# Kernel tuning notes

Hardware: AMD Instinct MI355X
Metric: run time of the kernel (lower is better)

Reference implementation:

```python
import jax, jax.numpy as jnp
import numpy as np

NUM_QUERIES = 300


def setup_inputs() -> dict:
    key = jax.random.key(0)
    ks = jax.random.split(key, 16)
    B, C, NC = 16, 256, 80
    s = 0.02
    return {
        "s3": jax.random.normal(ks[0], (B, C, 128, 128), jnp.float32),
        "s4": jax.random.normal(ks[1], (B, C, 64, 64), jnp.float32),
        "s5": jax.random.normal(ks[2], (B, C, 32, 32), jnp.float32),
        "w_score": jax.random.normal(ks[3], (C, NC), jnp.float32) * s,
        "b_score": jnp.zeros((NC,), jnp.float32),
        "w1": jax.random.normal(ks[4], (C, C), jnp.float32) * s,
        "b1": jnp.zeros((C,), jnp.float32),
        "w2": jax.random.normal(ks[5], (C, C), jnp.float32) * s,
        "b2": jnp.zeros((C,), jnp.float32),
        "w3": jax.random.normal(ks[6], (C, 4), jnp.float32) * s,
        "b3": jnp.zeros((4,), jnp.float32),
        "w_proj": jax.random.normal(ks[7], (C, C), jnp.float32) * s,
        "b_proj": jnp.zeros((C,), jnp.float32),
    }


def _flatten(feats):
    # each feat [B,C,H,W] -> [B,H*W,C]; concat over levels
    mems = [f.reshape(f.shape[0], f.shape[1], -1).transpose(0, 2, 1) for f in feats]
    return jnp.concatenate(mems, axis=1)


def reference(s3, s4, s5, w_score, b_score, w1, b1, w2, b2, w3, b3, w_proj, b_proj):
    memory = _flatten([s3, s4, s5])  # [B, N, C]

    # encoder heads
    enc_logits = memory @ w_score + b_score                      # [B, N, num_classes]
    h = jax.nn.relu(memory @ w1 + b1)
    h = jax.nn.relu(h @ w2 + b2)
    enc_boxes = h @ w3 + b3                                      # [B, N, 4]

    # top-k query selection: sigmoid -> per-token max class score -> topk -> gather
    scores = jax.nn.sigmoid(enc_logits).max(axis=-1)             # [B, N]
    topk_scores, topk_idx = jax.lax.top_k(scores, NUM_QUERIES)   # [B, K]
    topk_mem = jnp.take_along_axis(memory, topk_idx[:, :, None], axis=1)    # [B, K, C]
    topk_boxes = jnp.take_along_axis(enc_boxes, topk_idx[:, :, None], axis=1)  # [B, K, 4]

    tgt = topk_mem @ w_proj + b_proj                             # [B, K, C]
    ref_points = jax.nn.sigmoid(topk_boxes)                      # [B, K, 4]

    return (tgt, ref_points, enc_logits, jax.nn.sigmoid(enc_boxes), topk_idx, topk_scores)
```

## Files before the change

### kernel.cpp

```cpp
#include <hip/hip_runtime.h>
#include <math.h>

#define BATCH 16
#define CDIM 256
#define NCLS 80
#define N3 16384
#define N4 4096
#define N5 1024
#define NTOK 21504
#define KQ 300
#define KSEL 512
#define CANDMAX 1024

typedef __attribute__((ext_vector_type(8))) short short8;
typedef __attribute__((ext_vector_type(4))) float floatx4;
typedef unsigned short ushort_t;

__device__ __forceinline__ float sigmoidf_(float x) {
    return 1.0f / (1.0f + __expf(-x));
}

__device__ __forceinline__ ushort_t f2bf(float f) {
    unsigned int x = __float_as_uint(f);
    unsigned int r = (x + 0x7FFFu + ((x >> 16) & 1u)) >> 16;
    return (ushort_t)r;
}

__device__ __forceinline__ void locate_level(
    int n, int bb,
    const float* __restrict__ s3, const float* __restrict__ s4, const float* __restrict__ s5,
    const float*& src, int& nloc, int& lsz)
{
    if (n < N3)           { src = s3 + (size_t)bb * CDIM * N3; nloc = n;           lsz = N3; }
    else if (n < N3 + N4) { src = s4 + (size_t)bb * CDIM * N4; nloc = n - N3;      lsz = N4; }
    else                  { src = s5 + (size_t)bb * CDIM * N5; nloc = n - N3 - N4; lsz = N5; }
}

__global__ __launch_bounds__(256) void prep_weights(
    const float* __restrict__ w1, const float* __restrict__ w2,
    const float* __restrict__ w_score,
    ushort_t* __restrict__ w1T, ushort_t* __restrict__ w2T, ushort_t* __restrict__ wsT)
{
    const int k = threadIdx.x;
    const int c = blockIdx.x;
    if (c < 256) {
        w1T[c * 256 + k] = f2bf(w1[k * 256 + c]);
    } else if (c < 512) {
        const int c2 = c - 256;
        w2T[c2 * 256 + k] = f2bf(w2[k * 256 + c2]);
    } else {
        const int c2 = c - 512;
        wsT[c2 * 256 + k] = (c2 < NCLS) ? f2bf(w_score[k * NCLS + c2]) : (ushort_t)0;
    }
}

__global__ __launch_bounds__(256, 3) void enc_mfma_kernel(
    const float* __restrict__ s3, const float* __restrict__ s4, const float* __restrict__ s5,
    const ushort_t* __restrict__ w1T, const ushort_t* __restrict__ w2T,
    const ushort_t* __restrict__ wsT,
    const float* __restrict__ b_score, const float* __restrict__ b1,
    const float* __restrict__ b2,
    const float* __restrict__ w3, const float* __restrict__ b3,
    float* __restrict__ out_logits, float* __restrict__ out_sboxes,
    float* __restrict__ ws_scores)
{
    __shared__ __align__(16) ushort_t ldsA[256 * 68];
    __shared__ __align__(16) ushort_t wbuf[32][264];

    const int t = threadIdx.x;
    const int lane = t & 63;
    const int w = t >> 6;
    const int ml = lane & 15;
    const int quad = lane >> 4;
    const int kq = quad * 8;

    const int bb = blockIdx.x / 336;
    const int tile = blockIdx.x % 336;
    const int T0 = tile * 64;

    const float* src; int nloc, lsz;
    locate_level(T0, bb, s3, s4, s5, src, nloc, lsz);

    {
        const int tokq = t & 15;
        const int kr = t >> 4;
        #pragma unroll
        for (int p = 0; p < 16; ++p) {
            const int k = p * 16 + kr;
            const float4 v = *(const float4*)(src + (size_t)k * lsz + nloc + 4 * tokq);
            const unsigned int lo = (unsigned int)f2bf(v.x) | ((unsigned int)f2bf(v.y) << 16);
            const unsigned int hi = (unsigned int)f2bf(v.z) | ((unsigned int)f2bf(v.w) << 16);
            *(uint2*)&ldsA[k * 68 + 4 * tokq] = make_uint2(lo, hi);
        }
    }
    __syncthreads();

    short8 af[8];
    #pragma unroll
    for (int f = 0; f < 8; ++f) {
        short8 a;
        #pragma unroll
        for (int j = 0; j < 8; ++j)
            a[j] = (short)ldsA[(32 * f + kq + j) * 68 + 16 * w + ml];
        af[f] = a;
    }

    auto stage_w = [&](const ushort_t* wg) {
        #pragma unroll
        for (int s2 = 0; s2 < 4; ++s2) {
            const int idx = s2 * 256 + t;
            const int col = idx >> 5, ks = idx & 31;
            const short8 v = *(const short8*)(wg + (size_t)col * 256 + ks * 8);
            *(short8*)&wbuf[col][ks * 8] = v;
        }
    };

    const int tokg0 = bb * NTOK + T0 + 16 * w + quad * 4;
    const int tokl0 = 16 * w + quad * 4;

    float smax[4] = {-1e30f, -1e30f, -1e30f, -1e30f};
    for (int cc = 0; cc < 3; ++cc) {
        __syncthreads();
        stage_w(wsT + (size_t)cc * 32 * 256);
        __syncthreads();
        #pragma unroll
        for (int tt = 0; tt < 2; ++tt) {
            const int gt = cc * 2 + tt;
            if (gt >= 5) continue;
            floatx4 acc = {0.f, 0.f, 0.f, 0.f};
            #pragma unroll
            for (int f = 0; f < 8; ++f) {
                const short8 bf = *(const short8*)&wbuf[16 * tt + ml][32 * f + kq];
                acc = __builtin_amdgcn_mfma_f32_16x16x32_bf16(af[f], bf, acc, 0, 0, 0);
            }
            const int col = 16 * gt + ml;
            const float bias = b_score[col];
            #pragma unroll
            for (int r = 0; r < 4; ++r) {
                const float v = acc[r] + bias;
                out_logits[(size_t)(tokg0 + r) * NCLS + col] = v;
                smax[r] = fmaxf(smax[r], v);
            }
        }
    }
    #pragma unroll
    for (int r = 0; r < 4; ++r) {
        float m = smax[r];
        m = fmaxf(m, __shfl_xor(m, 1));
        m = fmaxf(m, __shfl_xor(m, 2));
        m = fmaxf(m, __shfl_xor(m, 4));
        m = fmaxf(m, __shfl_xor(m, 8));
        smax[r] = m;
    }
    if (ml == 0) {
        #pragma unroll
        for (int r = 0; r < 4; ++r)
            ws_scores[bb * NTOK + T0 + 16 * w + quad * 4 + r] = sigmoidf_(smax[r]);
    }

    for (int cc = 0; cc < 8; ++cc) {
        __syncthreads();
        stage_w(w1T + (size_t)cc * 32 * 256);
        __syncthreads();
        #pragma unroll
        for (int tt = 0; tt < 2; ++tt) {
            floatx4 acc = {0.f, 0.f, 0.f, 0.f};
            #pragma unroll
            for (int f = 0; f < 8; ++f) {
                const short8 bf = *(const short8*)&wbuf[16 * tt + ml][32 * f + kq];
                acc = __builtin_amdgcn_mfma_f32_16x16x32_bf16(af[f], bf, acc, 0, 0, 0);
            }
            const int col = 32 * cc + 16 * tt + ml;
            const float bias = b1[col];
            #pragma unroll
            for (int r = 0; r < 4; ++r) {
                const float v = fmaxf(acc[r] + bias, 0.f);
                ldsA[(tokl0 + r) * 264 + col] = f2bf(v);
            }
        }
    }
    __syncthreads();

    #pragma unroll
    for (int f = 0; f < 8; ++f)
        af[f] = *(const short8*)&ldsA[(16 * w + ml) * 264 + 32 * f + kq];

    float psum[4][4];
    #pragma unroll
    for (int r = 0; r < 4; ++r)
        #pragma unroll
        for (int c = 0; c < 4; ++c) psum[r][c] = 0.f;

    for (int cc = 0; cc < 8; ++cc) {
        __syncthreads();
        stage_w(w2T + (size_t)cc * 32 * 256);
        __syncthreads();
        #pragma unroll
        for (int tt = 0; tt < 2; ++tt) {
            floatx4 acc = {0.f, 0.f, 0.f, 0.f};
            #pragma unroll
            for (int f = 0; f < 8; ++f) {
                const short8 bf = *(const short8*)&wbuf[16 * tt + ml][32 * f + kq];
                acc = __builtin_amdgcn_mfma_f32_16x16x32_bf16(af[f], bf, acc, 0, 0, 0);
            }
            const int col = 32 * cc + 16 * tt + ml;
            const float bias = b2[col];
            const float4 w3v = *(const float4*)(w3 + col * 4);
            #pragma unroll
            for (int r = 0; r < 4; ++r) {
                const float v = fmaxf(acc[r] + bias, 0.f);
                psum[r][0] = fmaf(v, w3v.x, psum[r][0]);
                psum[r][1] = fmaf(v, w3v.y, psum[r][1]);
                psum[r][2] = fmaf(v, w3v.z, psum[r][2]);
                psum[r][3] = fmaf(v, w3v.w, psum[r][3]);
            }
        }
    }
    #pragma unroll
    for (int r = 0; r < 4; ++r)
        #pragma unroll
        for (int c = 0; c < 4; ++c) {
            float v = psum[r][c];
            v += __shfl_xor(v, 1);
            v += __shfl_xor(v, 2);
            v += __shfl_xor(v, 4);
            v += __shfl_xor(v, 8);
            psum[r][c] = v;
        }
    if (ml == 0) {
        #pragma unroll
        for (int r = 0; r < 4; ++r) {
            float4 o;
            o.x = sigmoidf_(psum[r][0] + b3[0]);
            o.y = sigmoidf_(psum[r][1] + b3[1]);
            o.z = sigmoidf_(psum[r][2] + b3[2]);
            o.w = sigmoidf_(psum[r][3] + b3[3]);
            *(float4*)&out_sboxes[(size_t)(bb * NTOK + T0 + 16 * w + quad * 4 + r) * 4] = o;
        }
    }
}

__global__ __launch_bounds__(256) void select_kernel(
    const float* __restrict__ scores,
    int* __restrict__ cand_idx, unsigned int* __restrict__ cand_cnt)
{
    const int bb = blockIdx.x;
    const int t = threadIdx.x;
    const float* s = scores + bb * NTOK;

    __shared__ unsigned int hist[256];
    __shared__ unsigned int prefix_s, cnt_s;

    unsigned int prefix = 0, mask = 0;
    int remaining = KSEL;
    for (int pass = 0; pass < 4; pass++) {
        const int shift = 24 - 8 * pass;
        hist[t] = 0;
        __syncthreads();
        for (int n = t; n < NTOK; n += 256) {
            unsigned int key = __float_as_uint(s[n]);
            if ((key & mask) == prefix) atomicAdd(&hist[(key >> shift) & 255u], 1u);
        }
        __syncthreads();
        if (t == 0) {
            int rem = remaining; unsigned int bsel = 0;
            for (int bin = 255; bin >= 0; bin--) {
                int c = (int)hist[bin];
                if (c >= rem) { bsel = (unsigned int)bin; break; }
                rem -= c;
            }
            prefix_s = prefix | (bsel << shift);
            hist[255] = (unsigned int)rem;
        }
        __syncthreads();
        prefix = prefix_s; remaining = (int)hist[255];
        mask |= 0xFFu << shift;
        __syncthreads();
    }
    const unsigned int Tkey = prefix;

    if (t == 0) cnt_s = 0;
    __syncthreads();
    for (int n = t; n < NTOK; n += 256) {
        unsigned int key = __float_as_uint(s[n]);
        if (key >= Tkey) {
            unsigned int pos = atomicAdd(&cnt_s, 1u);
            if (pos < CANDMAX) cand_idx[bb * CANDMAX + pos] = n;
        }
    }
    __syncthreads();
    if (t == 0) {
        unsigned int c = cnt_s; if (c > CANDMAX) c = CANDMAX;
        cand_cnt[bb] = c;
    }
}

__global__ __launch_bounds__(256) void rescore_kernel(
    const float* __restrict__ s3, const float* __restrict__ s4, const float* __restrict__ s5,
    const float* __restrict__ w_score, const float* __restrict__ b_score,
    const int* __restrict__ cand_idx, const unsigned int* __restrict__ cand_cnt,
    double* __restrict__ cand_score)
{
    __shared__ float mrow[4][CDIM];
    const int t = threadIdx.x;
    const int w = t >> 6;
    const int lane = t & 63;
    const int bb = blockIdx.x / (CANDMAX / 4);
    const int c  = (blockIdx.x % (CANDMAX / 4)) * 4 + w;
    const unsigned int cnt = cand_cnt[bb];
    const bool active = (unsigned int)c < cnt;

    int n = 0;
    if (active) n = cand_idx[bb * CANDMAX + c];
    if (active) {
        const float* src; int nloc, lsz;
        locate_level(n, bb, s3, s4, s5, src, nloc, lsz);
        #pragma unroll
        for (int j = 0; j < 4; j++)
            mrow[w][4 * lane + j] = src[(size_t)(4 * lane + j) * lsz + nloc];
    }
    __syncthreads();

    if (active) {
        double acc0 = (double)b_score[lane];
        double acc1 = (lane < 16) ? (double)b_score[64 + lane] : -1.0e300;
        for (int k = 0; k < CDIM; k++) {
            const double m = (double)mrow[w][k];
            acc0 += m * (double)w_score[k * NCLS + lane];
            if (lane < 16) acc1 += m * (double)w_score[k * NCLS + 64 + lane];
        }
        double mx = fmax(acc0, acc1);
        mx = fmax(mx, __shfl_xor(mx, 1));
        mx = fmax(mx, __shfl_xor(mx, 2));
        mx = fmax(mx, __shfl_xor(mx, 4));
        mx = fmax(mx, __shfl_xor(mx, 8));
        mx = fmax(mx, __shfl_xor(mx, 16));
        mx = fmax(mx, __shfl_xor(mx, 32));
        if (lane == 0) cand_score[bb * CANDMAX + c] = mx;
    }
}

__global__ __launch_bounds__(256) void fsort_kernel(
    const double* __restrict__ cand_score, const int* __restrict__ cand_idx,
    const unsigned int* __restrict__ cand_cnt,
    float* __restrict__ out_idx_f, float* __restrict__ out_scores,
    int* __restrict__ ws_idx)
{
    __shared__ double ss[CANDMAX];
    __shared__ int    ii[CANDMAX];
    const int bb = blockIdx.x;
    const int t = threadIdx.x;
    const unsigned int cnt = cand_cnt[bb];

    for (int i = t; i < CANDMAX; i += 256) {
        if ((unsigned int)i < cnt) {
            ss[i] = cand_score[bb * CANDMAX + i];
            ii[i] = cand_idx[bb * CANDMAX + i];
        } else {
            ss[i] = -1.0e300;
            ii[i] = 0x7FFFFFFF;
        }
    }
    __syncthreads();

    for (int ksz = 2; ksz <= CANDMAX; ksz <<= 1) {
        for (int j = ksz >> 1; j > 0; j >>= 1) {
            #pragma unroll
            for (int p = 0; p < CANDMAX / 256; p++) {
                const int i = p * 256 + t;
                const int ixj = i ^ j;
                if (ixj > i) {
                    double sa = ss[i], sb = ss[ixj];
                    int ia = ii[i], ib = ii[ixj];
                    const bool up = ((i & ksz) != 0);
                    const bool agtb = (sa > sb) || (sa == sb && ia < ib);
                    if (agtb == up) { ss[i] = sb; ss[ixj] = sa; ii[i] = ib; ii[ixj] = ia; }
                }
            }
            __syncthreads();
        }
    }

    for (int q = t; q < KQ; q += 256) {
        const double x = ss[q];
        const int idx = ii[q];
        out_scores[bb * KQ + q] = (float)(1.0 / (1.0 + exp(-x)));
        out_idx_f[bb * KQ + q] = (float)idx;
        ws_idx[bb * KQ + q] = idx;
    }
}

__global__ __launch_bounds__(256) void gather_proj_kernel(
    const float* __restrict__ s3, const float* __restrict__ s4, const float* __restrict__ s5,
    const float* __restrict__ w_proj, const float* __restrict__ b_proj,
    const int* __restrict__ ws_idx, const float* __restrict__ out_sboxes,
    float* __restrict__ out_tgt, float* __restrict__ out_ref)
{
    __shared__ float memQ[20][CDIM];
    __shared__ int qidx[20];
    const int t = threadIdx.x;
    const int bb = blockIdx.x / 15;
    const int tile = blockIdx.x % 15;
    const int q0 = tile * 20;

    if (t < 20) qidx[t] = ws_idx[bb * KQ + q0 + t];
    __syncthreads();

    #pragma unroll 4
    for (int q = 0; q < 20; q++) {
        const int n = qidx[q];
        const float* src; int nloc, lsz;
        locate_level(n, bb, s3, s4, s5, src, nloc, lsz);
        memQ[q][t] = src[(size_t)t * lsz + nloc];
    }
    __syncthreads();

    const int j = t;
    float acc[20];
    #pragma unroll
    for (int q = 0; q < 20; q++) acc[q] = b_proj[j];
    for (int k = 0; k < CDIM; k++) {
        const float w = w_proj[(size_t)k * CDIM + j];
        #pragma unroll
        for (int q = 0; q < 20; q++) acc[q] = fmaf(memQ[q][k], w, acc[q]);
    }
    #pragma unroll
    for (int q = 0; q < 20; q++)
        out_tgt[(size_t)(bb * KQ + q0 + q) * CDIM + j] = acc[q];

    if (t < 80) {
        const int q = t >> 2, c = t & 3;
        const int n = qidx[q];
        out_ref[(size_t)(bb * KQ + q0 + q) * 4 + c] =
            out_sboxes[(size_t)(bb * NTOK + n) * 4 + c];
    }
}

extern "C" void kernel_launch(void* const* d_in, const int* in_sizes, int n_in,
                              void* d_out, int out_size, void* d_ws, size_t ws_size,
                              hipStream_t stream) {
    const float* s3      = (const float*)d_in[0];
    const float* s4      = (const float*)d_in[1];
    const float* s5      = (const float*)d_in[2];
    const float* w_score = (const float*)d_in[3];
    const float* b_score = (const float*)d_in[4];
    const float* w1      = (const float*)d_in[5];
    const float* b1      = (const float*)d_in[6];
    const float* w2      = (const float*)d_in[7];
    const float* b2      = (const float*)d_in[8];
    const float* w3      = (const float*)d_in[9];
    const float* b3      = (const float*)d_in[10];
    const float* w_proj  = (const float*)d_in[11];
    const float* b_proj  = (const float*)d_in[12];

    float* out = (float*)d_out;
    float* out_tgt    = out;
    float* out_ref    = out + 1228800;
    float* out_logits = out + 1248000;
    float* out_sboxes = out + 28773120;
    float* out_idx    = out + 30149376;
    float* out_scores = out + 30154176;

    char* ws = (char*)d_ws;
    float*        ws_scores  = (float*)(ws + 0);
    double*       cand_score = (double*)(ws + 1376256);
    int*          cand_idx   = (int*)(ws + 1507328);
    unsigned int* cand_cnt   = (unsigned int*)(ws + 1572864);
    int*          ws_idx     = (int*)(ws + 1573120);
    ushort_t*     w1T        = (ushort_t*)(ws + 1592576);
    ushort_t*     w2T        = (ushort_t*)(ws + 1723648);
    ushort_t*     wsT        = (ushort_t*)(ws + 1854720);

    prep_weights<<<608, 256, 0, stream>>>(w1, w2, w_score, w1T, w2T, wsT);

    enc_mfma_kernel<<<BATCH * 336, 256, 0, stream>>>(
        s3, s4, s5, w1T, w2T, wsT, b_score, b1, b2, w3, b3,
        out_logits, out_sboxes, ws_scores);

    select_kernel<<<BATCH, 256, 0, stream>>>(ws_scores, cand_idx, cand_cnt);

    rescore_kernel<<<BATCH * (CANDMAX / 4), 256, 0, stream>>>(
        s3, s4, s5, w_score, b_score, cand_idx, cand_cnt, cand_score);

    fsort_kernel<<<BATCH, 256, 0, stream>>>(
        cand_score, cand_idx, cand_cnt, out_idx, out_scores, ws_idx);

    gather_proj_kernel<<<BATCH * 15, 256, 0, stream>>>(
        s3, s4, s5, w_proj, b_proj, ws_idx, out_sboxes, out_tgt, out_ref);
}
```

Before: 952.0 us.

## Double-buffer weight staging with async global-to-LDS loads and speed up selection

The encoder kernel now merges its three weight loops into one 19-step pipeline. It stages the next 32-column weight chunk into a second LDS buffer with global_load_lds while the current chunk feeds the MFMAs, and pre-swizzles the transposed weights to avoid LDS bank conflicts. Biases and w3 are cached in LDS, and the launch-bounds occupancy hint drops from 3 to 2 because LDS use grows. Separately, select_kernel moves to 1024 threads and uses wave-aggregated ballot atomics for the histogram and compaction. The candidate compaction order may now differ from before.

```diff
diff --git a/kernel.cpp b/kernel.cpp
--- a/kernel.cpp
+++ b/kernel.cpp
@@ -26,6 +26,13 @@
     return (ushort_t)r;
 }
 
+__device__ __forceinline__ void gload16(const void* g, void* l) {
+    __builtin_amdgcn_global_load_lds(
+        (const __attribute__((address_space(1))) unsigned int*)g,
+        (__attribute__((address_space(3))) unsigned int*)l,
+        16, 0, 0);
+}
+
 __device__ __forceinline__ void locate_level(
     int n, int bb,
     const float* __restrict__ s3, const float* __restrict__ s4, const float* __restrict__ s5,
@@ -43,18 +50,22 @@
 {
     const int k = threadIdx.x;
     const int c = blockIdx.x;
+    const int klo = k & 7;
     if (c < 256) {
-        w1T[c * 256 + k] = f2bf(w1[k * 256 + c]);
+        const size_t d = (size_t)c * 256 + ((((k >> 3) ^ (c & 7)) << 3) | klo);
+        w1T[d] = f2bf(w1[k * 256 + c]);
     } else if (c < 512) {
         const int c2 = c - 256;
-        w2T[c2 * 256 + k] = f2bf(w2[k * 256 + c2]);
+        const size_t d = (size_t)c2 * 256 + ((((k >> 3) ^ (c2 & 7)) << 3) | klo);
+        w2T[d] = f2bf(w2[k * 256 + c2]);
     } else {
         const int c2 = c - 512;
-        wsT[c2 * 256 + k] = (c2 < NCLS) ? f2bf(w_score[k * NCLS + c2]) : (ushort_t)0;
-    }
-}
-
-__global__ __launch_bounds__(256, 3) void enc_mfma_kernel(
+        const size_t d = (size_t)c2 * 256 + ((((k >> 3) ^ (c2 & 7)) << 3) | klo);
+        wsT[d] = (c2 < NCLS) ? f2bf(w_score[k * NCLS + c2]) : (ushort_t)0;
+    }
+}
+
+__global__ __launch_bounds__(256, 2) void enc_mfma_kernel(
     const float* __restrict__ s3, const float* __restrict__ s4, const float* __restrict__ s5,
     const ushort_t* __restrict__ w1T, const ushort_t* __restrict__ w2T,
     const ushort_t* __restrict__ wsT,
@@ -65,7 +76,11 @@
     float* __restrict__ ws_scores)
 {
     __shared__ __align__(16) ushort_t ldsA[256 * 68];
-    __shared__ __align__(16) ushort_t wbuf[32][264];
+    __shared__ __align__(16) ushort_t wbufL[2][32 * 256];
+    __shared__ float bsc_s[96];
+    __shared__ float b1_s[256];
+    __shared__ float b2_s[256];
+    __shared__ __align__(16) float w3_s[256 * 4];
 
     const int t = threadIdx.x;
     const int lane = t & 63;
@@ -73,10 +88,26 @@
     const int ml = lane & 15;
     const int quad = lane >> 4;
     const int kq = quad * 8;
+    const int m8 = ml & 7;
 
     const int bb = blockIdx.x / 336;
     const int tile = blockIdx.x % 336;
     const int T0 = tile * 64;
+
+    auto stage_async = [&](const ushort_t* wg, int dbuf) {
+        const char* g = (const char*)wg + w * 1024 + (lane << 4);
+        char* l = (char*)&wbufL[dbuf][0] + w * 1024;
+        #pragma unroll
+        for (int i = 0; i < 4; ++i)
+            gload16(g + i * 4096, l + i * 4096);
+    };
+
+    stage_async(wsT, 0);
+
+    if (t < 96) bsc_s[t] = b_score[t];
+    b1_s[t] = b1[t];
+    b2_s[t] = b2[t];
+    *(float4*)&w3_s[t * 4] = *(const float4*)(w3 + t * 4);
 
     const float* src; int nloc, lsz;
     locate_level(T0, bb, s3, s4, s5, src, nloc, lsz);
@@ -105,117 +136,96 @@
         af[f] = a;
     }
 
-    auto stage_w = [&](const ushort_t* wg) {
-        #pragma unroll
-        for (int s2 = 0; s2 < 4; ++s2) {
-            const int idx = s2 * 256 + t;
-            const int col = idx >> 5, ks = idx & 31;
-            const short8 v = *(const short8*)(wg + (size_t)col * 256 + ks * 8);
-            *(short8*)&wbuf[col][ks * 8] = v;
-        }
-    };
-
-    const int tokg0 = bb * NTOK + T0 + 16 * w + quad * 4;
     const int tokl0 = 16 * w + quad * 4;
+    const int tokg0 = bb * NTOK + T0 + tokl0;
 
     float smax[4] = {-1e30f, -1e30f, -1e30f, -1e30f};
-    for (int cc = 0; cc < 3; ++cc) {
-        __syncthreads();
-        stage_w(wsT + (size_t)cc * 32 * 256);
-        __syncthreads();
+    float psum[4][4];
+    #pragma unroll
+    for (int r = 0; r < 4; ++r)
+        #pragma unroll
+        for (int c = 0; c < 4; ++c) psum[r][c] = 0.f;
+
+    int cur = 0;
+    for (int i = 0; i < 19; ++i) {
+        if (i + 1 < 19) {
+            const int j = i + 1;
+            const ushort_t* nxt = (j < 3)  ? (wsT + (size_t)j * 8192)
+                                : (j < 11) ? (w1T + (size_t)(j - 3) * 8192)
+                                           : (w2T + (size_t)(j - 11) * 8192);
+            stage_async(nxt, cur ^ 1);
+        }
+
+        if (i == 11) {
+            #pragma unroll
+            for (int f = 0; f < 8; ++f)
+                af[f] = *(const short8*)&ldsA[(16 * w + ml) * 264 + 32 * f + kq];
+        }
+
+        const ushort_t* wb = &wbufL[cur][0];
         #pragma unroll
         for (int tt = 0; tt < 2; ++tt) {
-            const int gt = cc * 2 + tt;
-            if (gt >= 5) continue;
+            if (i < 3 && (2 * i + tt) >= 5) continue;
+            const int row = 16 * tt + ml;
             floatx4 acc = {0.f, 0.f, 0.f, 0.f};
             #pragma unroll
             for (int f = 0; f < 8; ++f) {
-                const short8 bf = *(const short8*)&wbuf[16 * tt + ml][32 * f + kq];
+                const short8 bf = *(const short8*)&wb[row * 256 + (((4 * f + quad) ^ m8) << 3)];
                 acc = __builtin_amdgcn_mfma_f32_16x16x32_bf16(af[f], bf, acc, 0, 0, 0);
             }
-            const int col = 16 * gt + ml;
-            const float bias = b_score[col];
+            if (i < 3) {
+                const int col = 16 * (2 * i + tt) + ml;
+                const float bias = bsc_s[col];
+                #pragma unroll
+                for (int r = 0; r < 4; ++r) {
+                    const float v = acc[r] + bias;
+                    out_logits[(size_t)(tokg0 + r) * NCLS + col] = v;
+                    smax[r] = fmaxf(smax[r], v);
+                }
+            } else if (i < 11) {
+                const int col = 32 * (i - 3) + 16 * tt + ml;
+                const float bias = b1_s[col];
+                #pragma unroll
+                for (int r = 0; r < 4; ++r) {
+                    const float v = fmaxf(acc[r] + bias, 0.f);
+                    ldsA[(tokl0 + r) * 264 + col] = f2bf(v);
+                }
+            } else {
+                const int col = 32 * (i - 11) + 16 * tt + ml;
+                const float bias = b2_s[col];
+                const float4 w3v = *(const float4*)&w3_s[col * 4];
+                #pragma unroll
+                for (int r = 0; r < 4; ++r) {
+                    const float v = fmaxf(acc[r] + bias, 0.f);
+                    psum[r][0] = fmaf(v, w3v.x, psum[r][0]);
+                    psum[r][1] = fmaf(v, w3v.y, psum[r][1]);
+                    psum[r][2] = fmaf(v, w3v.z, psum[r][2]);
+                    psum[r][3] = fmaf(v, w3v.w, psum[r][3]);
+                }
+            }
+        }
+
+        if (i == 2) {
             #pragma unroll
             for (int r = 0; r < 4; ++r) {
-                const float v = acc[r] + bias;
-                out_logits[(size_t)(tokg0 + r) * NCLS + col] = v;
-                smax[r] = fmaxf(smax[r], v);
-            }
-        }
-    }
-    #pragma unroll
-    for (int r = 0; r < 4; ++r) {
-        float m = smax[r];
-        m = fmaxf(m, __shfl_xor(m, 1));
-        m = fmaxf(m, __shfl_xor(m, 2));
-        m = fmaxf(m, __shfl_xor(m, 4));
-        m = fmaxf(m, __shfl_xor(m, 8));
-        smax[r] = m;
-    }
-    if (ml == 0) {
-        #pragma unroll
-        for (int r = 0; r < 4; ++r)
-            ws_scores[bb * NTOK + T0 + 16 * w + quad * 4 + r] = sigmoidf_(smax[r]);
-    }
-
-    for (int cc = 0; cc < 8; ++cc) {
+                float m = smax[r];
+                m = fmaxf(m, __shfl_xor(m, 1));
+                m = fmaxf(m, __shfl_xor(m, 2));
+                m = fmaxf(m, __shfl_xor(m, 4));
+                m = fmaxf(m, __shfl_xor(m, 8));
+                smax[r] = m;
+            }
+            if (ml == 0) {
+                #pragma unroll
+                for (int r = 0; r < 4; ++r)
+                    ws_scores[bb * NTOK + T0 + 16 * w + quad * 4 + r] = sigmoidf_(smax[r]);
+            }
+        }
+
         __syncthreads();
-        stage_w(w1T + (size_t)cc * 32 * 256);
-        __syncthreads();
-        #pragma unroll
-        for (int tt = 0; tt < 2; ++tt) {
-            floatx4 acc = {0.f, 0.f, 0.f, 0.f};
-            #pragma unroll
-            for (int f = 0; f < 8; ++f) {
-                const short8 bf = *(const short8*)&wbuf[16 * tt + ml][32 * f + kq];
-                acc = __builtin_amdgcn_mfma_f32_16x16x32_bf16(af[f], bf, acc, 0, 0, 0);
-            }
-            const int col = 32 * cc + 16 * tt + ml;
-            const float bias = b1[col];
-            #pragma unroll
-            for (int r = 0; r < 4; ++r) {
-                const float v = fmaxf(acc[r] + bias, 0.f);
-                ldsA[(tokl0 + r) * 264 + col] = f2bf(v);
-            }
-        }
-    }
-    __syncthreads();
-
-    #pragma unroll
-    for (int f = 0; f < 8; ++f)
-        af[f] = *(const short8*)&ldsA[(16 * w + ml) * 264 + 32 * f + kq];
-
-    float psum[4][4];
-    #pragma unroll
-    for (int r = 0; r < 4; ++r)
-        #pragma unroll
-        for (int c = 0; c < 4; ++c) psum[r][c] = 0.f;
-
-    for (int cc = 0; cc < 8; ++cc) {
-        __syncthreads();
-        stage_w(w2T + (size_t)cc * 32 * 256);
-        __syncthreads();
-        #pragma unroll
-        for (int tt = 0; tt < 2; ++tt) {
-            floatx4 acc = {0.f, 0.f, 0.f, 0.f};
-            #pragma unroll
-            for (int f = 0; f < 8; ++f) {
-                const short8 bf = *(const short8*)&wbuf[16 * tt + ml][32 * f + kq];
-                acc = __builtin_amdgcn_mfma_f32_16x16x32_bf16(af[f], bf, acc, 0, 0, 0);
-            }
-            const int col = 32 * cc + 16 * tt + ml;
-            const float bias = b2[col];
-            const float4 w3v = *(const float4*)(w3 + col * 4);
-            #pragma unroll
-            for (int r = 0; r < 4; ++r) {
-                const float v = fmaxf(acc[r] + bias, 0.f);
-                psum[r][0] = fmaf(v, w3v.x, psum[r][0]);
-                psum[r][1] = fmaf(v, w3v.y, psum[r][1]);
-                psum[r][2] = fmaf(v, w3v.z, psum[r][2]);
-                psum[r][3] = fmaf(v, w3v.w, psum[r][3]);
-            }
-        }
-    }
+        cur ^= 1;
+    }
+
     #pragma unroll
     for (int r = 0; r < 4; ++r)
         #pragma unroll
@@ -240,26 +250,37 @@
     }
 }
 
-__global__ __launch_bounds__(256) void select_kernel(
+__global__ __launch_bounds__(1024) void select_kernel(
     const float* __restrict__ scores,
     int* __restrict__ cand_idx, unsigned int* __restrict__ cand_cnt)
 {
     const int bb = blockIdx.x;
     const int t = threadIdx.x;
+    const int lane = t & 63;
     const float* s = scores + bb * NTOK;
 
     __shared__ unsigned int hist[256];
-    __shared__ unsigned int prefix_s, cnt_s;
+    __shared__ unsigned int prefix_s, rem_s, cnt_s;
 
     unsigned int prefix = 0, mask = 0;
     int remaining = KSEL;
     for (int pass = 0; pass < 4; pass++) {
         const int shift = 24 - 8 * pass;
-        hist[t] = 0;
+        if (t < 256) hist[t] = 0;
         __syncthreads();
-        for (int n = t; n < NTOK; n += 256) {
-            unsigned int key = __float_as_uint(s[n]);
-            if ((key & mask) == prefix) atomicAdd(&hist[(key >> shift) & 255u], 1u);
+        for (int n = t; n < NTOK; n += 1024) {
+            const unsigned int key = __float_as_uint(s[n]);
+            const bool pred = ((key & mask) == prefix);
+            const unsigned int bin = (key >> shift) & 255u;
+            unsigned long long alive = __ballot(pred);
+            while (alive) {
+                const int leader = __builtin_ctzll(alive);
+                const unsigned int lbin = (unsigned int)__shfl((int)bin, leader);
+                const unsigned long long match = alive & __ballot(bin == lbin);
+                if (lane == leader)
+                    atomicAdd(&hist[lbin], (unsigned int)__popcll(match));
+                alive &= ~match;
+            }
         }
         __syncthreads();
         if (t == 0) {
@@ -270,10 +291,10 @@
                 rem -= c;
             }
             prefix_s = prefix | (bsel << shift);
-            hist[255] = (unsigned int)rem;
+            rem_s = (unsigned int)rem;
         }
         __syncthreads();
-        prefix = prefix_s; remaining = (int)hist[255];
+        prefix = prefix_s; remaining = (int)rem_s;
         mask |= 0xFFu << shift;
         __syncthreads();
     }
@@ -281,11 +302,20 @@
 
     if (t == 0) cnt_s = 0;
     __syncthreads();
-    for (int n = t; n < NTOK; n += 256) {
-        unsigned int key = __float_as_uint(s[n]);
-        if (key >= Tkey) {
-            unsigned int pos = atomicAdd(&cnt_s, 1u);
-            if (pos < CANDMAX) cand_idx[bb * CANDMAX + pos] = n;
+    for (int n = t; n < NTOK; n += 1024) {
+        const unsigned int key = __float_as_uint(s[n]);
+        const bool pred = (key >= Tkey);
+        const unsigned long long m = __ballot(pred);
+        if (m) {
+            const int leader = __builtin_ctzll(m);
+            unsigned int base = 0;
+            if (lane == leader) base = atomicAdd(&cnt_s, (unsigned int)__popcll(m));
+            base = (unsigned int)__shfl((int)base, leader);
+            if (pred) {
+                const unsigned int pos =
+                    base + (unsigned int)__popcll(m & ((1ull << lane) - 1ull));
+                if (pos < CANDMAX) cand_idx[bb * CANDMAX + pos] = n;
+            }
         }
     }
     __syncthreads();
@@ -477,7 +507,7 @@
         s3, s4, s5, w1T, w2T, wsT, b_score, b1, b2, w3, b3,
         out_logits, out_sboxes, ws_scores);
 
-    select_kernel<<<BATCH, 256, 0, stream>>>(ws_scores, cand_idx, cand_cnt);
+    select_kernel<<<BATCH, 1024, 0, stream>>>(ws_scores, cand_idx, cand_cnt);
 
     rescore_kernel<<<BATCH * (CANDMAX / 4), 256, 0, stream>>>(
         s3, s4, s5, w_score, b_score, cand_idx, cand_cnt, cand_score);
```

Measured after the change: 956.4 us. No clear change (+0.5%).
